# Performance work log

Hardware: AMD Instinct MI355X
Metric: run time of the kernel (lower is better)

The kernel has to match this reference:

```python
import jax, jax.numpy as jnp
import numpy as np

D_MODEL = 256; D_FFN = 1024; N_LEVELS = 4; N_HEADS = 8; N_POINTS = 4; N_VT = 8
D_HEAD = D_MODEL // N_HEADS
SHAPES = [(64, 64), (32, 32), (16, 16), (8, 8)]
L_SP = sum(h * w for h, w in SHAPES)  # 5440
BATCH = 4
EPS = 1e-5


def _ln(x, g, b):
    m = jnp.mean(x, -1, keepdims=True)
    xc = x - m
    v = jnp.mean(xc * xc, -1, keepdims=True)
    return g * xc * jax.lax.rsqrt(v + EPS) + b


def _bilinear(v_flat, x, y, H, W):
    # v_flat: (N, H*W, M, Dh); x, y: (N, Q, M) pixel coords (align_corners=False, zero padding)
    x0 = jnp.floor(x); y0 = jnp.floor(y)
    wx = x - x0; wy = y - y0
    out = 0.0
    for cx, cy, w in ((x0, y0, (1 - wx) * (1 - wy)), (x0 + 1, y0, wx * (1 - wy)),
                      (x0, y0 + 1, (1 - wx) * wy), (x0 + 1, y0 + 1, wx * wy)):
        valid = (cx >= 0) & (cx < W) & (cy >= 0) & (cy < H)
        xi = jnp.clip(cx, 0, W - 1).astype(jnp.int32)
        yi = jnp.clip(cy, 0, H - 1).astype(jnp.int32)
        idx = (yi * W + xi)[..., None]  # (N, Q, M, 1)
        g = jnp.take_along_axis(v_flat, idx, axis=1)  # (N, Q, M, Dh)
        out = out + (w * valid)[..., None] * g
    return out


def _msdeform_attn(query, ref, value_in, shapes_np, pad_mask, Wv, bv, Wo, bo, Wa, ba, Wp, bp):
    N, Lq, D = query.shape
    M, Lv, P, Dh = N_HEADS, N_LEVELS, N_POINTS, D_HEAD
    value = value_in @ Wv.T + bv
    value = jnp.where(pad_mask[..., None], 0.0, value)
    value = value.reshape(N, Lq, M, Dh)
    off = (query @ Wo.T + bo).reshape(N, Lq, M, Lv, P, 2)
    attn = jax.nn.softmax((query @ Wa.T + ba).reshape(N, Lq, M, Lv * P), axis=-1)
    attn = attn.reshape(N, Lq, M, Lv, P)
    # offset normalizer is (W, H) per level
    normalizer = jnp.asarray([[w, h] for h, w in shapes_np], jnp.float32)
    loc = ref[:, :, None, :, None, :] + off / normalizer[None, None, None, :, None, :]
    out = 0.0
    start = 0
    for l, (H, W) in enumerate(shapes_np):
        v_l = value[:, start:start + H * W]  # (N, H*W, M, Dh)
        x = (loc[:, :, :, l, :, 0] * W - 0.5).transpose(0, 1, 3, 2).reshape(N, Lq * P, M)
        y = (loc[:, :, :, l, :, 1] * H - 0.5).transpose(0, 1, 3, 2).reshape(N, Lq * P, M)
        samp = _bilinear(v_l, x, y, H, W).reshape(N, Lq, P, M, Dh)
        out = out + jnp.einsum('nqpmd,nqmp->nqmd', samp, attn[:, :, :, l, :])
        start += H * W
    return out.reshape(N, Lq, D) @ Wp.T + bp


def setup_inputs() -> dict:
    key = jax.random.key(0)
    ks = jax.random.split(key, 16)
    N, D = BATCH, D_MODEL
    Lq = L_SP + N_VT
    s = D ** -0.5
    rn = lambda k, sh, sc=1.0: jax.random.normal(k, sh, dtype=jnp.float32) * sc
    starts = np.cumsum([0] + [h * w for h, w in SHAPES[:-1]])
    return {
        'src': rn(ks[0], (N, L_SP, D)),
        'pos': rn(ks[1], (N, L_SP, D), 0.1),
        'reference_points': jax.random.uniform(ks[2], (N, Lq, N_LEVELS, 2), dtype=jnp.float32),
        'spatial_shapes': jnp.asarray(SHAPES, jnp.int32),
        'level_start_index': jnp.asarray(starts, jnp.int32),
        'padding_mask': jnp.zeros((N, Lq), bool),
        'all_vt': rn(ks[3], (N, 75 * N_VT, D)),
        'sel_vt': rn(ks[4], (N, N_VT, D)),
        'W_value': rn(ks[5], (D, D), s), 'b_value': jnp.zeros((D,), jnp.float32),
        'W_off': rn(ks[6], (N_HEADS * N_LEVELS * N_POINTS * 2, D), s),
        'b_off': rn(ks[7], (N_HEADS * N_LEVELS * N_POINTS * 2,), 0.1),
        'W_attn': rn(ks[8], (N_HEADS * N_LEVELS * N_POINTS, D), s),
        'b_attn': jnp.zeros((N_HEADS * N_LEVELS * N_POINTS,), jnp.float32),
        'W_out': rn(ks[9], (D, D), s), 'b_out': jnp.zeros((D,), jnp.float32),
        'g1': jnp.ones((D,), jnp.float32), 'beta1': jnp.zeros((D,), jnp.float32),
        'W1': rn(ks[10], (D_FFN, D), s), 'bf1': jnp.zeros((D_FFN,), jnp.float32),
        'W2': rn(ks[11], (D, D_FFN), D_FFN ** -0.5), 'bf2': jnp.zeros((D,), jnp.float32),
        'g2': jnp.ones((D,), jnp.float32), 'beta2': jnp.zeros((D,), jnp.float32),
    }


def reference(src, pos, reference_points, spatial_shapes, level_start_index, padding_mask,
              all_vt, sel_vt, W_value, b_value, W_off, b_off, W_attn, b_attn, W_out, b_out,
              g1, beta1, W1, bf1, W2, bf2, g2, beta2):
    shapes_np = [tuple(int(v) for v in row) for row in np.asarray(spatial_shapes)]
    q = jnp.concatenate([src + pos, sel_vt], axis=1)      # (N, Lq, D)
    v_in = jnp.concatenate([src, sel_vt], axis=1)
    src2 = _msdeform_attn(q, reference_points, v_in, shapes_np, padding_mask,
                          W_value, b_value, W_off, b_off, W_attn, b_attn, W_out, b_out)
    x = _ln(v_in + src2, g1, beta1)
    h = jax.nn.relu(x @ W1.T + bf1) @ W2.T + bf2
    x = _ln(x + h, g2, beta2)
    return (x[:, :L_SP, :], all_vt, x[:, L_SP:, :])
```

## Files before the change

kernel.cpp:

```cpp
#include <hip/hip_runtime.h>
#include <math.h>

#define NB   4
#define LQ   5448
#define LSP  5440
#define NR   21792
#define DM   256

typedef unsigned short u16;
typedef __attribute__((ext_vector_type(8))) short short8;
typedef __attribute__((ext_vector_type(4))) float f32x4;
typedef __attribute__((ext_vector_type(4))) unsigned int uint4v;

__device__ __forceinline__ u16 f2bf(float f) {
  unsigned int u = __float_as_uint(f);
  u = (u + 0x7fff + ((u >> 16) & 1)) >> 16;
  return (u16)u;
}
__device__ __forceinline__ float bf2f(u16 u) {
  return __uint_as_float(((unsigned int)u) << 16);
}
__device__ __forceinline__ uint4v pack8(float4 a, float4 b) {
  uint4v r;
  r.x = (unsigned)f2bf(a.x) | ((unsigned)f2bf(a.y) << 16);
  r.y = (unsigned)f2bf(a.z) | ((unsigned)f2bf(a.w) << 16);
  r.z = (unsigned)f2bf(b.x) | ((unsigned)f2bf(b.y) << 16);
  r.w = (unsigned)f2bf(b.z) | ((unsigned)f2bf(b.w) << 16);
  return r;
}

#define OFF_R0 0ull
#define OFF_R1 44630016ull
#define OFF_R2 55787520ull
#define OFF_R3 66945024ull
#define OFF_WB 78102528ull
#define OFF_BI 79609856ull

#define WOF_V  0
#define WOF_OA 65536
#define WOF_P  163840
#define WOF_1  229376
#define WOF_2  491520
#define NWELEM 753664

#define OUT0 5570560ull
#define OUT1 614400ull

__global__ __launch_bounds__(256) void convw_k(
    const float* __restrict__ Wv, const float* __restrict__ Wo,
    const float* __restrict__ Wa, const float* __restrict__ Wp,
    const float* __restrict__ W1, const float* __restrict__ W2,
    const float* __restrict__ bo, const float* __restrict__ ba,
    u16* __restrict__ out, float* __restrict__ boa)
{
  const int gid = blockIdx.x * 256 + threadIdx.x;
  if (gid < 384) boa[gid] = (gid < 256) ? bo[gid] : ba[gid - 256];
  if (gid >= NWELEM) return;
  float v;
  if (gid < WOF_OA) {
    v = Wv[gid];
  } else if (gid < WOF_P) {
    const int o = gid - WOF_OA;
    v = (o < 65536) ? Wo[o] : Wa[o - 65536];
  } else if (gid < WOF_1) {
    v = Wp[gid - WOF_P];
  } else if (gid < WOF_2) {
    v = W1[gid - WOF_1];
  } else {
    v = W2[gid - WOF_2];
  }
  out[gid] = f2bf(v);
}

template <int AMODE, int EPI, int BN>
__global__ __launch_bounds__(BN) void gemmP(
    const u16* __restrict__ A, int lda,
    const float* __restrict__ src, const float* __restrict__ pos,
    const float* __restrict__ sel,
    const u16* __restrict__ B, int ldb,
    const float* __restrict__ bias, int K,
    u16* __restrict__ outb, int ldob,
    const u16* __restrict__ xbf,
    const float* __restrict__ gvec, const float* __restrict__ bvec,
    float* __restrict__ outf, int ldof)
{
  constexpr int NW = BN / 64;
  __shared__ u16 As[64 * 256];
  __shared__ u16 Bs[NW * 4096];
  const int tid = threadIdx.x;
  const int w = tid >> 6, lane = tid & 63;
  const int l15 = lane & 15, quad = lane >> 4;
  const int m0 = blockIdx.y * 64;
  const int n0 = blockIdx.x * BN;
  const int swz = (quad ^ ((l15 >> 1) & 3)) * 8;

  const int rA = (tid & 255) >> 2;
  const int pA = tid & 3;
  const int cA = (pA ^ ((rA >> 1) & 3)) * 8;
  const int ldsA = rA * 32 + pA * 8;
  int gmA = m0 + rA; if (gmA >= NR) gmA = NR - 1;
  const float* aV = nullptr; const float* aP = nullptr;
  if (AMODE) {
    const int n = gmA / LQ, i = gmA - n * LQ;
    if (i < LSP) {
      aV = src + ((size_t)(n * LSP + i)) * DM;
      if (AMODE == 1) aP = pos + ((size_t)(n * LSP + i)) * DM;
    } else {
      aV = sel + ((size_t)(n * 8 + (i - LSP))) * DM;
    }
  }

  int rB[4], cB[4], lB[4];
#pragma unroll
  for (int i = 0; i < 4; ++i) {
    const int g = lane + i * 64;
    rB[i] = g >> 2;
    const int p = g & 3;
    cB[i] = (p ^ ((rB[i] >> 1) & 3)) * 8;
    lB[i] = w * 4096 + rB[i] * 32 + p * 8;
  }
  const u16* Brow = B + (size_t)(n0 + w * 64) * ldb;

  f32x4 acc[4][4] = {};

  for (int kc = 0; kc < K; kc += 256) {
    if (kc) __syncthreads();
    if (tid < 256) {
      if (AMODE == 0) {
        const u16* ap = A + (size_t)gmA * lda + kc + cA;
#pragma unroll
        for (int i = 0; i < 8; i += 4) {
          uint4v t0 = *(const uint4v*)(ap + (i + 0) * 32);
          uint4v t1 = *(const uint4v*)(ap + (i + 1) * 32);
          uint4v t2 = *(const uint4v*)(ap + (i + 2) * 32);
          uint4v t3 = *(const uint4v*)(ap + (i + 3) * 32);
          *(uint4v*)&As[(i + 0) * 2048 + ldsA] = t0;
          *(uint4v*)&As[(i + 1) * 2048 + ldsA] = t1;
          *(uint4v*)&As[(i + 2) * 2048 + ldsA] = t2;
          *(uint4v*)&As[(i + 3) * 2048 + ldsA] = t3;
        }
      } else {
#pragma unroll
        for (int i = 0; i < 8; i += 2) {
          float4 v0a = *(const float4*)(aV + (i + 0) * 32 + cA);
          float4 v0b = *(const float4*)(aV + (i + 0) * 32 + cA + 4);
          float4 v1a = *(const float4*)(aV + (i + 1) * 32 + cA);
          float4 v1b = *(const float4*)(aV + (i + 1) * 32 + cA + 4);
          if (AMODE == 1 && aP) {
            const float4 p0a = *(const float4*)(aP + (i + 0) * 32 + cA);
            const float4 p0b = *(const float4*)(aP + (i + 0) * 32 + cA + 4);
            const float4 p1a = *(const float4*)(aP + (i + 1) * 32 + cA);
            const float4 p1b = *(const float4*)(aP + (i + 1) * 32 + cA + 4);
            v0a.x += p0a.x; v0a.y += p0a.y; v0a.z += p0a.z; v0a.w += p0a.w;
            v0b.x += p0b.x; v0b.y += p0b.y; v0b.z += p0b.z; v0b.w += p0b.w;
            v1a.x += p1a.x; v1a.y += p1a.y; v1a.z += p1a.z; v1a.w += p1a.w;
            v1b.x += p1b.x; v1b.y += p1b.y; v1b.z += p1b.z; v1b.w += p1b.w;
          }
          *(uint4v*)&As[(i + 0) * 2048 + ldsA] = pack8(v0a, v0b);
          *(uint4v*)&As[(i + 1) * 2048 + ldsA] = pack8(v1a, v1b);
        }
      }
    }
    __syncthreads();

    uint4v rb0[4], rb1[4];
#pragma unroll
    for (int i = 0; i < 4; ++i)
      rb0[i] = *(const uint4v*)(Brow + (size_t)rB[i] * ldb + kc + cB[i]);
#pragma unroll
    for (int i = 0; i < 4; ++i)
      rb1[i] = *(const uint4v*)(Brow + (size_t)rB[i] * ldb + kc + 32 + cB[i]);
#pragma unroll
    for (int i = 0; i < 4; ++i) *(uint4v*)&Bs[lB[i]] = rb0[i];

#pragma unroll
    for (int j = 0; j < 8; ++j) {
      if (j < 6) {
        if ((j & 1) == 0) {
#pragma unroll
          for (int i = 0; i < 4; ++i)
            rb0[i] = *(const uint4v*)(Brow + (size_t)rB[i] * ldb + kc + (j + 2) * 32 + cB[i]);
        } else {
#pragma unroll
          for (int i = 0; i < 4; ++i)
            rb1[i] = *(const uint4v*)(Brow + (size_t)rB[i] * ldb + kc + (j + 2) * 32 + cB[i]);
        }
      }
      short8 af[4], bfr[4];
#pragma unroll
      for (int r = 0; r < 4; ++r)
        af[r] = *(const short8*)&As[j * 2048 + (r * 16 + l15) * 32 + swz];
#pragma unroll
      for (int c = 0; c < 4; ++c)
        bfr[c] = *(const short8*)&Bs[w * 4096 + (j & 1) * 2048 + (c * 16 + l15) * 32 + swz];
      if (j < 7) {
        const int buf = ((j + 1) & 1) * 2048;
        if ((j & 1) == 0) {
#pragma unroll
          for (int i = 0; i < 4; ++i) *(uint4v*)&Bs[lB[i] + buf] = rb1[i];
        } else {
#pragma unroll
          for (int i = 0; i < 4; ++i) *(uint4v*)&Bs[lB[i] + buf] = rb0[i];
        }
      }
#pragma unroll
      for (int r = 0; r < 4; ++r)
#pragma unroll
        for (int c = 0; c < 4; ++c)
          acc[r][c] = __builtin_amdgcn_mfma_f32_16x16x32_bf16(af[r], bfr[c], acc[r][c], 0, 0, 0);
    }
  }

  int col[4];
  float bb[4];
#pragma unroll
  for (int c = 0; c < 4; ++c) {
    col[c] = n0 + w * 64 + c * 16 + l15;
    bb[c] = bias[col[c]];
  }

  if (EPI == 4) {
#pragma unroll
    for (int c = 0; c < 4; ++c)
#pragma unroll
      for (int r = 0; r < 4; ++r)
#pragma unroll
        for (int j = 0; j < 4; ++j) {
          const int row = m0 + r * 16 + quad * 4 + j;
          if (row < NR) outf[(size_t)row * ldof + col[c]] = acc[r][c][j] + bb[c];
        }
    return;
  }

  if (EPI <= 1) {
#pragma unroll
    for (int c = 0; c < 4; ++c)
#pragma unroll
      for (int r = 0; r < 4; ++r)
#pragma unroll
        for (int j = 0; j < 4; ++j) {
          const int row = m0 + r * 16 + quad * 4 + j;
          if (row < NR) {
            float v = acc[r][c][j] + bb[c];
            if (EPI == 1) v = fmaxf(v, 0.f);
            outb[(size_t)row * ldob + col[c]] = f2bf(v);
          }
        }
    return;
  }

  __syncthreads();
  float sv[4][4], sq[4][4];
#pragma unroll
  for (int r = 0; r < 4; ++r) {
#pragma unroll
    for (int j = 0; j < 4; ++j) {
      const int row = m0 + r * 16 + quad * 4 + j;
      const int rc = (row < NR) ? row : NR - 1;
      if (EPI == 2) {
        const int n = rc / LQ;
        const int i = rc - n * LQ;
        const float* resb = (i < LSP)
            ? src + ((size_t)(n * LSP + i)) * DM
            : sel + ((size_t)(n * 8 + (i - LSP))) * DM;
#pragma unroll
        for (int c = 0; c < 4; ++c) acc[r][c][j] += bb[c] + resb[col[c]];
      } else {
#pragma unroll
        for (int c = 0; c < 4; ++c)
          acc[r][c][j] += bb[c] + bf2f(xbf[(size_t)rc * DM + col[c]]);
      }
      float s = 0.f, q = 0.f;
#pragma unroll
      for (int c = 0; c < 4; ++c) {
        const float v = acc[r][c][j];
        s += v; q += v * v;
      }
      sv[r][j] = s; sq[r][j] = q;
    }
  }
#pragma unroll
  for (int off = 1; off < 16; off <<= 1) {
#pragma unroll
    for (int r = 0; r < 4; ++r)
#pragma unroll
      for (int j = 0; j < 4; ++j) {
        sv[r][j] += __shfl_xor(sv[r][j], off, 64);
        sq[r][j] += __shfl_xor(sq[r][j], off, 64);
      }
  }
  float* red = (float*)As;
  if (l15 == 0) {
#pragma unroll
    for (int r = 0; r < 4; ++r)
#pragma unroll
      for (int j = 0; j < 4; ++j) {
        const int rl = r * 16 + quad * 4 + j;
        red[(rl * 4 + w) * 2 + 0] = sv[r][j];
        red[(rl * 4 + w) * 2 + 1] = sq[r][j];
      }
  }
  __syncthreads();

  float gg[4], b2[4];
#pragma unroll
  for (int c = 0; c < 4; ++c) { gg[c] = gvec[col[c]]; b2[c] = bvec[col[c]]; }

#pragma unroll
  for (int r = 0; r < 4; ++r) {
#pragma unroll
    for (int j = 0; j < 4; ++j) {
      const int row = m0 + r * 16 + quad * 4 + j;
      if (row >= NR) continue;
      const int rl = r * 16 + quad * 4 + j;
      float ms = 0.f, mq = 0.f;
#pragma unroll
      for (int ww = 0; ww < 4; ++ww) {
        ms += red[(rl * 4 + ww) * 2 + 0];
        mq += red[(rl * 4 + ww) * 2 + 1];
      }
      const float mean = ms * (1.f / 256.f);
      const float var = mq * (1.f / 256.f) - mean * mean;
      const float rin = rsqrtf(var + 1e-5f);
      if (EPI == 2) {
#pragma unroll
        for (int c = 0; c < 4; ++c)
          outb[(size_t)row * DM + col[c]] =
              f2bf(gg[c] * (acc[r][c][j] - mean) * rin + b2[c]);
      } else {
        const int n = row / LQ;
        const int i = row - n * LQ;
        float* dst = (i < LSP)
            ? outf + (size_t)(n * LSP + i) * DM
            : outf + OUT0 + OUT1 + (size_t)(n * 8 + (i - LSP)) * DM;
#pragma unroll
        for (int c = 0; c < 4; ++c)
          dst[col[c]] = gg[c] * (acc[r][c][j] - mean) * rin + b2[c];
      }
    }
  }
}

__device__ __forceinline__ void acc8(float* a, const u16* p, float w) {
  const uint4v u = *(const uint4v*)p;
  a[0] += w * __uint_as_float((u.x & 0xffffu) << 16);
  a[1] += w * __uint_as_float(u.x & 0xffff0000u);
  a[2] += w * __uint_as_float((u.y & 0xffffu) << 16);
  a[3] += w * __uint_as_float(u.y & 0xffff0000u);
  a[4] += w * __uint_as_float((u.z & 0xffffu) << 16);
  a[5] += w * __uint_as_float(u.z & 0xffff0000u);
  a[6] += w * __uint_as_float((u.w & 0xffffu) << 16);
  a[7] += w * __uint_as_float(u.w & 0xffff0000u);
}

__global__ __launch_bounds__(256) void sample3_k(
    const u16* __restrict__ value, const float* __restrict__ oa,
    const float* __restrict__ ref, u16* __restrict__ samp)
{
  const int lb = blockIdx.x;
  const int xcd = lb & 7;
  const int idx = lb >> 3;
  const int batch = xcd >> 1;
  const int rg = idx * 2 + (xcd & 1);
  if (rg >= 681) return;
  const int lane = threadIdx.x & 63;
  const int li = threadIdx.x & 31;
  const int m = li >> 2, q4 = li & 3;
  const int row = batch * LQ + rg * 8 + (threadIdx.x >> 5);

  const float* oar = oa + (size_t)row * 384;
  const float* offm = oar + m * 32;

  const float4 lg = *(const float4*)(oar + 256 + m * 16 + q4 * 4);
  float mx = fmaxf(fmaxf(lg.x, lg.y), fmaxf(lg.z, lg.w));
  mx = fmaxf(mx, __shfl_xor(mx, 1, 64));
  mx = fmaxf(mx, __shfl_xor(mx, 2, 64));
  const float e0 = __expf(lg.x - mx), e1 = __expf(lg.y - mx),
              e2 = __expf(lg.z - mx), e3 = __expf(lg.w - mx);
  float s = e0 + e1 + e2 + e3;
  s += __shfl_xor(s, 1, 64);
  s += __shfl_xor(s, 2, 64);
  const float inv = 1.f / s;
  float wp[4] = {e0 * inv, e1 * inv, e2 * inv, e3 * inv};

  const float4 r01 = *(const float4*)(ref + (size_t)row * 8);
  const float4 r23 = *(const float4*)(ref + (size_t)row * 8 + 4);
  const float RX[4] = {r01.x, r01.z, r23.x, r23.z};
  const float RY[4] = {r01.y, r01.w, r23.y, r23.w};
  const int HW[4] = {64, 32, 16, 8};
  const int ST[4] = {0, 4096, 5120, 5376};

  float a[8] = {};
#pragma unroll
  for (int l = 0; l < 4; ++l) {
    const int W = HW[l], H = HW[l];
    const float rx = RX[l], ry = RY[l];
    const u16* vb = value + ((size_t)(batch * LQ + ST[l])) * DM + m * 32 + q4 * 8;
    const float4 oA = *(const float4*)(offm + l * 8);
    const float4 oB = *(const float4*)(offm + l * 8 + 4);
    const float ox[4] = {oA.x, oA.z, oB.x, oB.z};
    const float oy[4] = {oA.y, oA.w, oB.y, oB.w};
#pragma unroll
    for (int p = 0; p < 4; ++p) {
      const float aw = __shfl(wp[p], (lane & ~3) | l, 64);
      const float px = rx * (float)W + ox[p] - 0.5f;
      const float py = ry * (float)H + oy[p] - 0.5f;
      const float xf = floorf(px), yf = floorf(py);
      const float wx = px - xf, wy = py - yf;
      const int x0 = (int)xf, y0 = (int)yf;
      const int x1 = x0 + 1, y1 = y0 + 1;
      const bool vx0 = (x0 >= 0) & (x0 < W), vx1 = (x1 >= 0) & (x1 < W);
      const bool vy0 = (y0 >= 0) & (y0 < H), vy1 = (y1 >= 0) & (y1 < H);
      if (vy0 & vx0) acc8(a, vb + (size_t)(y0 * W + x0) * DM, aw * (1.f - wx) * (1.f - wy));
      if (vy0 & vx1) acc8(a, vb + (size_t)(y0 * W + x1) * DM, aw * wx * (1.f - wy));
      if (vy1 & vx0) acc8(a, vb + (size_t)(y1 * W + x0) * DM, aw * (1.f - wx) * wy);
      if (vy1 & vx1) acc8(a, vb + (size_t)(y1 * W + x1) * DM, aw * wx * wy);
    }
  }
  uint4v ov;
  ov.x = (unsigned int)f2bf(a[0]) | ((unsigned int)f2bf(a[1]) << 16);
  ov.y = (unsigned int)f2bf(a[2]) | ((unsigned int)f2bf(a[3]) << 16);
  ov.z = (unsigned int)f2bf(a[4]) | ((unsigned int)f2bf(a[5]) << 16);
  ov.w = (unsigned int)f2bf(a[6]) | ((unsigned int)f2bf(a[7]) << 16);
  *(uint4v*)(samp + (size_t)row * DM + m * 32 + q4 * 8) = ov;
}

extern "C" void kernel_launch(void* const* d_in, const int* in_sizes, int n_in,
                              void* d_out, int out_size, void* d_ws, size_t ws_size,
                              hipStream_t stream)
{
  const float* src = (const float*)d_in[0];
  const float* pos = (const float*)d_in[1];
  const float* ref = (const float*)d_in[2];
  const float* all_vt = (const float*)d_in[6];
  const float* sel = (const float*)d_in[7];
  const float* Wv = (const float*)d_in[8];
  const float* bv = (const float*)d_in[9];
  const float* Wo = (const float*)d_in[10];
  const float* bo = (const float*)d_in[11];
  const float* Wa = (const float*)d_in[12];
  const float* ba = (const float*)d_in[13];
  const float* Wp = (const float*)d_in[14];
  const float* bp = (const float*)d_in[15];
  const float* g1 = (const float*)d_in[16];
  const float* be1 = (const float*)d_in[17];
  const float* W1 = (const float*)d_in[18];
  const float* b1 = (const float*)d_in[19];
  const float* W2 = (const float*)d_in[20];
  const float* b2 = (const float*)d_in[21];
  const float* g2 = (const float*)d_in[22];
  const float* be2 = (const float*)d_in[23];

  char* ws = (char*)d_ws;
  float* oabuf = (float*)(ws + OFF_R0);
  u16* h_bf    = (u16*)(ws + OFF_R0);
  u16* samp_bf = (u16*)(ws + OFF_R1);
  u16* x_bf    = (u16*)(ws + OFF_R2);
  u16* val_bf  = (u16*)(ws + OFF_R3);
  u16* WB      = (u16*)(ws + OFF_WB);
  float* boa   = (float*)(ws + OFF_BI);

  const dim3 b256(256), b384(384);
  const int MT64 = (NR + 63) / 64;

  convw_k<<<dim3(NWELEM / 256), b256, 0, stream>>>(
      Wv, Wo, Wa, Wp, W1, W2, bo, ba, WB, boa);
  gemmP<2, 0, 256><<<dim3(1, MT64), b256, 0, stream>>>(
      nullptr, 0, src, nullptr, sel, WB + WOF_V, 256, bv, 256,
      val_bf, 256, nullptr, nullptr, nullptr, nullptr, 0);
  gemmP<1, 4, 384><<<dim3(1, MT64), b384, 0, stream>>>(
      nullptr, 0, src, pos, sel, WB + WOF_OA, 256, boa, 256,
      nullptr, 0, nullptr, nullptr, nullptr, oabuf, 384);
  sample3_k<<<dim3(8 * 341), b256, 0, stream>>>(val_bf, oabuf, ref, samp_bf);
  gemmP<0, 2, 256><<<dim3(1, MT64), b256, 0, stream>>>(
      samp_bf, 256, src, nullptr, sel, WB + WOF_P, 256, bp, 256,
      x_bf, 256, nullptr, g1, be1, nullptr, 0);
  gemmP<0, 1, 256><<<dim3(4, MT64), b256, 0, stream>>>(
      x_bf, 256, nullptr, nullptr, nullptr, WB + WOF_1, 256, b1, 256,
      h_bf, 1024, nullptr, nullptr, nullptr, nullptr, 0);
  gemmP<0, 3, 256><<<dim3(1, MT64), b256, 0, stream>>>(
      h_bf, 1024, nullptr, nullptr, nullptr, WB + WOF_2, 1024, b2, 1024,
      nullptr, 0, x_bf, g2, be2, (float*)d_out, 0);
  hipMemcpyAsync((float*)d_out + OUT0, all_vt, OUT1 * sizeof(float),
                 hipMemcpyDeviceToDevice, stream);
}
```

Before: 317.5 us.

## Use direct global-to-LDS loads in GEMMs and batch sampler gathers

The GEMM kernel is rewritten to stage A and B tiles with global_load_lds (direct global-to-LDS DMA) in 128-wide K chunks instead of register-staged double buffering. The offset/attention GEMM now uses 256 threads with 6 column tiles per wave instead of 384 threads. The bilinear sampler computes all 16 clamped indices and masked weights per level first, then issues 16 independent gathers before accumulating, to increase memory-level parallelism. Risks include losing the previous software pipelining of B loads, and extra loads for out-of-bounds corners that are now fetched with zero weight.

```diff
diff --git a/kernel.cpp b/kernel.cpp
--- a/kernel.cpp
+++ b/kernel.cpp
@@ -27,6 +27,12 @@
   r.z = (unsigned)f2bf(b.x) | ((unsigned)f2bf(b.y) << 16);
   r.w = (unsigned)f2bf(b.z) | ((unsigned)f2bf(b.w) << 16);
   return r;
+}
+
+__device__ __forceinline__ void gld_lds16(const u16* g, u16* l) {
+  __builtin_amdgcn_global_load_lds(
+      (const __attribute__((address_space(1))) void*)g,
+      (__attribute__((address_space(3))) void*)l, 16, 0, 0);
 }
 
 #define OFF_R0 0ull
@@ -72,8 +78,8 @@
   out[gid] = f2bf(v);
 }
 
-template <int AMODE, int EPI, int BN>
-__global__ __launch_bounds__(BN) void gemmP(
+template <int AMODE, int EPI, int WC>
+__global__ __launch_bounds__(256) void gemmF(
     const u16* __restrict__ A, int lda,
     const float* __restrict__ src, const float* __restrict__ pos,
     const float* __restrict__ sel,
@@ -84,24 +90,27 @@
     const float* __restrict__ gvec, const float* __restrict__ bvec,
     float* __restrict__ outf, int ldof)
 {
-  constexpr int NW = BN / 64;
-  __shared__ u16 As[64 * 256];
-  __shared__ u16 Bs[NW * 4096];
+  constexpr int BN = WC * 64;
+  __shared__ u16 As[4 * 64 * 32];
+  __shared__ u16 Bs[4 * BN * 32];
   const int tid = threadIdx.x;
   const int w = tid >> 6, lane = tid & 63;
   const int l15 = lane & 15, quad = lane >> 4;
   const int m0 = blockIdx.y * 64;
   const int n0 = blockIdx.x * BN;
   const int swz = (quad ^ ((l15 >> 1) & 3)) * 8;
-
-  const int rA = (tid & 255) >> 2;
-  const int pA = tid & 3;
+  const int ga8 = ((lane & 3) ^ ((lane >> 3) & 3)) * 8;
+  const int seglane = lane >> 2;
+
+  int gmA = m0 + w * 16 + seglane; if (gmA >= NR) gmA = NR - 1;
+
+  const int rA = tid >> 2, pA = tid & 3;
   const int cA = (pA ^ ((rA >> 1) & 3)) * 8;
   const int ldsA = rA * 32 + pA * 8;
-  int gmA = m0 + rA; if (gmA >= NR) gmA = NR - 1;
-  const float* aV = nullptr; const float* aP = nullptr;
+  const float *aV = nullptr, *aP = nullptr;
   if (AMODE) {
-    const int n = gmA / LQ, i = gmA - n * LQ;
+    int gm = m0 + rA; if (gm >= NR) gm = NR - 1;
+    const int n = gm / LQ, i = gm - n * LQ;
     if (i < LSP) {
       aV = src + ((size_t)(n * LSP + i)) * DM;
       if (AMODE == 1) aP = pos + ((size_t)(n * LSP + i)) * DM;
@@ -110,118 +119,84 @@
     }
   }
 
-  int rB[4], cB[4], lB[4];
-#pragma unroll
-  for (int i = 0; i < 4; ++i) {
-    const int g = lane + i * 64;
-    rB[i] = g >> 2;
-    const int p = g & 3;
-    cB[i] = (p ^ ((rB[i] >> 1) & 3)) * 8;
-    lB[i] = w * 4096 + rB[i] * 32 + p * 8;
-  }
-  const u16* Brow = B + (size_t)(n0 + w * 64) * ldb;
-
-  f32x4 acc[4][4] = {};
-
-  for (int kc = 0; kc < K; kc += 256) {
+  f32x4 acc[4][WC] = {};
+
+  for (int kc = 0; kc < K; kc += 128) {
     if (kc) __syncthreads();
-    if (tid < 256) {
-      if (AMODE == 0) {
-        const u16* ap = A + (size_t)gmA * lda + kc + cA;
-#pragma unroll
-        for (int i = 0; i < 8; i += 4) {
-          uint4v t0 = *(const uint4v*)(ap + (i + 0) * 32);
-          uint4v t1 = *(const uint4v*)(ap + (i + 1) * 32);
-          uint4v t2 = *(const uint4v*)(ap + (i + 2) * 32);
-          uint4v t3 = *(const uint4v*)(ap + (i + 3) * 32);
-          *(uint4v*)&As[(i + 0) * 2048 + ldsA] = t0;
-          *(uint4v*)&As[(i + 1) * 2048 + ldsA] = t1;
-          *(uint4v*)&As[(i + 2) * 2048 + ldsA] = t2;
-          *(uint4v*)&As[(i + 3) * 2048 + ldsA] = t3;
+    float4 av[4][2], pv[4][2];
+    if (AMODE) {
+#pragma unroll
+      for (int kt = 0; kt < 4; ++kt) {
+        av[kt][0] = *(const float4*)(aV + kc + kt * 32 + cA);
+        av[kt][1] = *(const float4*)(aV + kc + kt * 32 + cA + 4);
+      }
+      if (AMODE == 1) {
+        if (aP) {
+#pragma unroll
+          for (int kt = 0; kt < 4; ++kt) {
+            pv[kt][0] = *(const float4*)(aP + kc + kt * 32 + cA);
+            pv[kt][1] = *(const float4*)(aP + kc + kt * 32 + cA + 4);
+          }
+        } else {
+#pragma unroll
+          for (int kt = 0; kt < 4; ++kt) {
+            pv[kt][0] = make_float4(0.f, 0.f, 0.f, 0.f);
+            pv[kt][1] = make_float4(0.f, 0.f, 0.f, 0.f);
+          }
         }
-      } else {
-#pragma unroll
-        for (int i = 0; i < 8; i += 2) {
-          float4 v0a = *(const float4*)(aV + (i + 0) * 32 + cA);
-          float4 v0b = *(const float4*)(aV + (i + 0) * 32 + cA + 4);
-          float4 v1a = *(const float4*)(aV + (i + 1) * 32 + cA);
-          float4 v1b = *(const float4*)(aV + (i + 1) * 32 + cA + 4);
-          if (AMODE == 1 && aP) {
-            const float4 p0a = *(const float4*)(aP + (i + 0) * 32 + cA);
-            const float4 p0b = *(const float4*)(aP + (i + 0) * 32 + cA + 4);
-            const float4 p1a = *(const float4*)(aP + (i + 1) * 32 + cA);
-            const float4 p1b = *(const float4*)(aP + (i + 1) * 32 + cA + 4);
-            v0a.x += p0a.x; v0a.y += p0a.y; v0a.z += p0a.z; v0a.w += p0a.w;
-            v0b.x += p0b.x; v0b.y += p0b.y; v0b.z += p0b.z; v0b.w += p0b.w;
-            v1a.x += p1a.x; v1a.y += p1a.y; v1a.z += p1a.z; v1a.w += p1a.w;
-            v1b.x += p1b.x; v1b.y += p1b.y; v1b.z += p1b.z; v1b.w += p1b.w;
-          }
-          *(uint4v*)&As[(i + 0) * 2048 + ldsA] = pack8(v0a, v0b);
-          *(uint4v*)&As[(i + 1) * 2048 + ldsA] = pack8(v1a, v1b);
+      }
+    }
+#pragma unroll
+    for (int kt = 0; kt < 4; ++kt) {
+      if (AMODE == 0)
+        gld_lds16(A + (size_t)gmA * lda + kc + kt * 32 + ga8,
+                  &As[kt * 2048 + w * 512]);
+      for (int s = w; s < BN / 16; s += 4)
+        gld_lds16(B + (size_t)(n0 + s * 16 + seglane) * ldb + kc + kt * 32 + ga8,
+                  &Bs[kt * BN * 32 + s * 512]);
+    }
+    if (AMODE) {
+#pragma unroll
+      for (int kt = 0; kt < 4; ++kt) {
+        float4 a0 = av[kt][0], a1 = av[kt][1];
+        if (AMODE == 1) {
+          a0.x += pv[kt][0].x; a0.y += pv[kt][0].y;
+          a0.z += pv[kt][0].z; a0.w += pv[kt][0].w;
+          a1.x += pv[kt][1].x; a1.y += pv[kt][1].y;
+          a1.z += pv[kt][1].z; a1.w += pv[kt][1].w;
         }
+        *(uint4v*)&As[kt * 2048 + ldsA] = pack8(a0, a1);
       }
     }
     __syncthreads();
-
-    uint4v rb0[4], rb1[4];
-#pragma unroll
-    for (int i = 0; i < 4; ++i)
-      rb0[i] = *(const uint4v*)(Brow + (size_t)rB[i] * ldb + kc + cB[i]);
-#pragma unroll
-    for (int i = 0; i < 4; ++i)
-      rb1[i] = *(const uint4v*)(Brow + (size_t)rB[i] * ldb + kc + 32 + cB[i]);
-#pragma unroll
-    for (int i = 0; i < 4; ++i) *(uint4v*)&Bs[lB[i]] = rb0[i];
-
-#pragma unroll
-    for (int j = 0; j < 8; ++j) {
-      if (j < 6) {
-        if ((j & 1) == 0) {
-#pragma unroll
-          for (int i = 0; i < 4; ++i)
-            rb0[i] = *(const uint4v*)(Brow + (size_t)rB[i] * ldb + kc + (j + 2) * 32 + cB[i]);
-        } else {
-#pragma unroll
-          for (int i = 0; i < 4; ++i)
-            rb1[i] = *(const uint4v*)(Brow + (size_t)rB[i] * ldb + kc + (j + 2) * 32 + cB[i]);
-        }
-      }
-      short8 af[4], bfr[4];
+#pragma unroll
+    for (int kt = 0; kt < 4; ++kt) {
+      short8 af[4], bfr[WC];
 #pragma unroll
       for (int r = 0; r < 4; ++r)
-        af[r] = *(const short8*)&As[j * 2048 + (r * 16 + l15) * 32 + swz];
-#pragma unroll
-      for (int c = 0; c < 4; ++c)
-        bfr[c] = *(const short8*)&Bs[w * 4096 + (j & 1) * 2048 + (c * 16 + l15) * 32 + swz];
-      if (j < 7) {
-        const int buf = ((j + 1) & 1) * 2048;
-        if ((j & 1) == 0) {
-#pragma unroll
-          for (int i = 0; i < 4; ++i) *(uint4v*)&Bs[lB[i] + buf] = rb1[i];
-        } else {
-#pragma unroll
-          for (int i = 0; i < 4; ++i) *(uint4v*)&Bs[lB[i] + buf] = rb0[i];
-        }
-      }
+        af[r] = *(const short8*)&As[kt * 2048 + (r * 16 + l15) * 32 + swz];
+#pragma unroll
+      for (int c = 0; c < WC; ++c)
+        bfr[c] = *(const short8*)&Bs[kt * BN * 32 + (w * WC * 16 + c * 16 + l15) * 32 + swz];
 #pragma unroll
       for (int r = 0; r < 4; ++r)
 #pragma unroll
-        for (int c = 0; c < 4; ++c)
+        for (int c = 0; c < WC; ++c)
           acc[r][c] = __builtin_amdgcn_mfma_f32_16x16x32_bf16(af[r], bfr[c], acc[r][c], 0, 0, 0);
     }
   }
 
-  int col[4];
-  float bb[4];
-#pragma unroll
-  for (int c = 0; c < 4; ++c) {
-    col[c] = n0 + w * 64 + c * 16 + l15;
+  int col[WC];
+  float bb[WC];
+#pragma unroll
+  for (int c = 0; c < WC; ++c) {
+    col[c] = n0 + w * WC * 16 + c * 16 + l15;
     bb[c] = bias[col[c]];
   }
 
   if (EPI == 4) {
 #pragma unroll
-    for (int c = 0; c < 4; ++c)
+    for (int c = 0; c < WC; ++c)
 #pragma unroll
       for (int r = 0; r < 4; ++r)
 #pragma unroll
@@ -234,7 +209,7 @@
 
   if (EPI <= 1) {
 #pragma unroll
-    for (int c = 0; c < 4; ++c)
+    for (int c = 0; c < WC; ++c)
 #pragma unroll
       for (int r = 0; r < 4; ++r)
 #pragma unroll
@@ -264,15 +239,15 @@
             ? src + ((size_t)(n * LSP + i)) * DM
             : sel + ((size_t)(n * 8 + (i - LSP))) * DM;
 #pragma unroll
-        for (int c = 0; c < 4; ++c) acc[r][c][j] += bb[c] + resb[col[c]];
+        for (int c = 0; c < WC; ++c) acc[r][c][j] += bb[c] + resb[col[c]];
       } else {
 #pragma unroll
-        for (int c = 0; c < 4; ++c)
+        for (int c = 0; c < WC; ++c)
           acc[r][c][j] += bb[c] + bf2f(xbf[(size_t)rc * DM + col[c]]);
       }
       float s = 0.f, q = 0.f;
 #pragma unroll
-      for (int c = 0; c < 4; ++c) {
+      for (int c = 0; c < WC; ++c) {
         const float v = acc[r][c][j];
         s += v; q += v * v;
       }
@@ -302,9 +277,9 @@
   }
   __syncthreads();
 
-  float gg[4], b2[4];
-#pragma unroll
-  for (int c = 0; c < 4; ++c) { gg[c] = gvec[col[c]]; b2[c] = bvec[col[c]]; }
+  float gg[WC], b2[WC];
+#pragma unroll
+  for (int c = 0; c < WC; ++c) { gg[c] = gvec[col[c]]; b2[c] = bvec[col[c]]; }
 
 #pragma unroll
   for (int r = 0; r < 4; ++r) {
@@ -324,7 +299,7 @@
       const float rin = rsqrtf(var + 1e-5f);
       if (EPI == 2) {
 #pragma unroll
-        for (int c = 0; c < 4; ++c)
+        for (int c = 0; c < WC; ++c)
           outb[(size_t)row * DM + col[c]] =
               f2bf(gg[c] * (acc[r][c][j] - mean) * rin + b2[c]);
       } else {
@@ -334,15 +309,14 @@
             ? outf + (size_t)(n * LSP + i) * DM
             : outf + OUT0 + OUT1 + (size_t)(n * 8 + (i - LSP)) * DM;
 #pragma unroll
-        for (int c = 0; c < 4; ++c)
+        for (int c = 0; c < WC; ++c)
           dst[col[c]] = gg[c] * (acc[r][c][j] - mean) * rin + b2[c];
       }
     }
   }
 }
 
-__device__ __forceinline__ void acc8(float* a, const u16* p, float w) {
-  const uint4v u = *(const uint4v*)p;
+__device__ __forceinline__ void acc8w(float* a, const uint4v u, float w) {
   a[0] += w * __uint_as_float((u.x & 0xffffu) << 16);
   a[1] += w * __uint_as_float(u.x & 0xffff0000u);
   a[2] += w * __uint_as_float((u.y & 0xffffu) << 16);
@@ -353,7 +327,7 @@
   a[7] += w * __uint_as_float(u.w & 0xffff0000u);
 }
 
-__global__ __launch_bounds__(256) void sample3_k(
+__global__ __launch_bounds__(256) void sample4_k(
     const u16* __restrict__ value, const float* __restrict__ oa,
     const float* __restrict__ ref, u16* __restrict__ samp)
 {
@@ -393,29 +367,44 @@
   float a[8] = {};
 #pragma unroll
   for (int l = 0; l < 4; ++l) {
-    const int W = HW[l], H = HW[l];
+    const int W = HW[l];
     const float rx = RX[l], ry = RY[l];
     const u16* vb = value + ((size_t)(batch * LQ + ST[l])) * DM + m * 32 + q4 * 8;
     const float4 oA = *(const float4*)(offm + l * 8);
     const float4 oB = *(const float4*)(offm + l * 8 + 4);
     const float ox[4] = {oA.x, oA.z, oB.x, oB.z};
     const float oy[4] = {oA.y, oA.w, oB.y, oB.w};
+    int idx16[16];
+    float wt16[16];
 #pragma unroll
     for (int p = 0; p < 4; ++p) {
       const float aw = __shfl(wp[p], (lane & ~3) | l, 64);
       const float px = rx * (float)W + ox[p] - 0.5f;
-      const float py = ry * (float)H + oy[p] - 0.5f;
+      const float py = ry * (float)W + oy[p] - 0.5f;
       const float xf = floorf(px), yf = floorf(py);
       const float wx = px - xf, wy = py - yf;
       const int x0 = (int)xf, y0 = (int)yf;
       const int x1 = x0 + 1, y1 = y0 + 1;
-      const bool vx0 = (x0 >= 0) & (x0 < W), vx1 = (x1 >= 0) & (x1 < W);
-      const bool vy0 = (y0 >= 0) & (y0 < H), vy1 = (y1 >= 0) & (y1 < H);
-      if (vy0 & vx0) acc8(a, vb + (size_t)(y0 * W + x0) * DM, aw * (1.f - wx) * (1.f - wy));
-      if (vy0 & vx1) acc8(a, vb + (size_t)(y0 * W + x1) * DM, aw * wx * (1.f - wy));
-      if (vy1 & vx0) acc8(a, vb + (size_t)(y1 * W + x0) * DM, aw * (1.f - wx) * wy);
-      if (vy1 & vx1) acc8(a, vb + (size_t)(y1 * W + x1) * DM, aw * wx * wy);
-    }
+      const int x0c = min(max(x0, 0), W - 1), x1c = min(max(x1, 0), W - 1);
+      const int y0c = min(max(y0, 0), W - 1), y1c = min(max(y1, 0), W - 1);
+      const bool vx0 = (x0 == x0c), vx1 = (x1 == x1c);
+      const bool vy0 = (y0 == y0c), vy1 = (y1 == y1c);
+      const float wxa = aw * wx, wxb = aw * (1.f - wx);
+      wt16[p * 4 + 0] = (vx0 & vy0) ? wxb * (1.f - wy) : 0.f;
+      wt16[p * 4 + 1] = (vx1 & vy0) ? wxa * (1.f - wy) : 0.f;
+      wt16[p * 4 + 2] = (vx0 & vy1) ? wxb * wy : 0.f;
+      wt16[p * 4 + 3] = (vx1 & vy1) ? wxa * wy : 0.f;
+      idx16[p * 4 + 0] = y0c * W + x0c;
+      idx16[p * 4 + 1] = y0c * W + x1c;
+      idx16[p * 4 + 2] = y1c * W + x0c;
+      idx16[p * 4 + 3] = y1c * W + x1c;
+    }
+    uint4v d[16];
+#pragma unroll
+    for (int i = 0; i < 16; ++i)
+      d[i] = *(const uint4v*)(vb + (size_t)idx16[i] * DM);
+#pragma unroll
+    for (int i = 0; i < 16; ++i) acc8w(a, d[i], wt16[i]);
   }
   uint4v ov;
   ov.x = (unsigned int)f2bf(a[0]) | ((unsigned int)f2bf(a[1]) << 16);
@@ -460,25 +449,25 @@
   u16* WB      = (u16*)(ws + OFF_WB);
   float* boa   = (float*)(ws + OFF_BI);
 
-  const dim3 b256(256), b384(384);
+  const dim3 b256(256);
   const int MT64 = (NR + 63) / 64;
 
   convw_k<<<dim3(NWELEM / 256), b256, 0, stream>>>(
       Wv, Wo, Wa, Wp, W1, W2, bo, ba, WB, boa);
-  gemmP<2, 0, 256><<<dim3(1, MT64), b256, 0, stream>>>(
+  gemmF<2, 0, 4><<<dim3(1, MT64), b256, 0, stream>>>(
       nullptr, 0, src, nullptr, sel, WB + WOF_V, 256, bv, 256,
       val_bf, 256, nullptr, nullptr, nullptr, nullptr, 0);
-  gemmP<1, 4, 384><<<dim3(1, MT64), b384, 0, stream>>>(
+  gemmF<1, 4, 6><<<dim3(1, MT64), b256, 0, stream>>>(
       nullptr, 0, src, pos, sel, WB + WOF_OA, 256, boa, 256,
       nullptr, 0, nullptr, nullptr, nullptr, oabuf, 384);
-  sample3_k<<<dim3(8 * 341), b256, 0, stream>>>(val_bf, oabuf, ref, samp_bf);
-  gemmP<0, 2, 256><<<dim3(1, MT64), b256, 0, stream>>>(
+  sample4_k<<<dim3(8 * 341), b256, 0, stream>>>(val_bf, oabuf, ref, samp_bf);
+  gemmF<0, 2, 4><<<dim3(1, MT64), b256, 0, stream>>>(
       samp_bf, 256, src, nullptr, sel, WB + WOF_P, 256, bp, 256,
       x_bf, 256, nullptr, g1, be1, nullptr, 0);
-  gemmP<0, 1, 256><<<dim3(4, MT64), b256, 0, stream>>>(
+  gemmF<0, 1, 4><<<dim3(4, MT64), b256, 0, stream>>>(
       x_bf, 256, nullptr, nullptr, nullptr, WB + WOF_1, 256, b1, 256,
       h_bf, 1024, nullptr, nullptr, nullptr, nullptr, 0);
-  gemmP<0, 3, 256><<<dim3(1, MT64), b256, 0, stream>>>(
+  gemmF<0, 3, 4><<<dim3(1, MT64), b256, 0, stream>>>(
       h_bf, 1024, nullptr, nullptr, nullptr, WB + WOF_2, 1024, b2, 1024,
       nullptr, 0, x_bf, g2, be2, (float*)d_out, 0);
   hipMemcpyAsync((float*)d_out + OUT0, all_vt, OUT1 * sizeof(float),
```

Result: slower. 393.2 us (+23.9%).
